# Optimization experiments

Hardware: AMD Instinct MI355X
Metric: run time of the kernel (lower is better)

Reference implementation:

```python
import jax, jax.numpy as jnp
import numpy as np

BZ, T, D, DFF, E, BEAMS = 128, 32, 768, 3072, 8, 2


def setup_inputs() -> dict:
    key = jax.random.key(0)
    ks = jax.random.split(key, 4)
    s = 0.02
    return {
        "x": jax.random.normal(ks[0], (BZ, T, D), jnp.float32),
        "attention_mask": jnp.ones((BZ, T), jnp.float32),
        "Wg": jax.random.normal(ks[1], (D, E), jnp.float32) * s,   # gate Linear(D,E,bias=False)
        "W1": jax.random.normal(ks[2], (E, D, DFF), jnp.float32) * s,
        "b1": jnp.zeros((E, DFF), jnp.float32),
        "W2": jax.random.normal(ks[3], (E, DFF, D), jnp.float32) * s,
        "b2": jnp.zeros((E, D), jnp.float32),
    }


def reference(x, attention_mask, Wg, W1, b1, W2, b2):
    # forward_gate: module builds its own all-ones mask regardless of input mask
    mask = jnp.ones((x.shape[0], x.shape[1]), x.dtype)
    x_avg = (x * mask[..., None]).sum(1) / mask[..., None].sum(1)   # [bz, D]
    prob = jax.nn.softmax(x_avg @ Wg, axis=-1)                       # [bz, E]
    # beam_search (layer_judge='first', pre-route): topk on exp(log(softmax)) == softmax probs
    scores = jnp.exp(jnp.log(prob))
    topv, topi = jax.lax.top_k(scores, BEAMS)                        # [bz, beams]
    beam_scores = topv.reshape(-1)                                   # [bz*beams]
    expert_route = topi.reshape(-1, 1)                                # [bz*beams, 1]
    sel = expert_route[:, -1]
    # replicate x per beam: [bz*beams, T, D]
    x_rep = jnp.broadcast_to(x[:, None], (x.shape[0], BEAMS, x.shape[1], x.shape[2]))
    x_rep = x_rep.reshape(-1, x.shape[1], x.shape[2])
    # per-sample expert FFN dispatch (dense masked loop over the E=8 experts)
    out = jnp.zeros_like(x_rep)
    for e in range(E):
        h = jax.nn.gelu(jnp.einsum('nsd,df->nsf', x_rep, W1[e]) + b1[e], approximate=False)
        ye = jnp.einsum('nsf,fd->nsd', h, W2[e]) + b2[e]
        out = jnp.where((sel == e)[:, None, None], ye, out)
    return (out, beam_scores, expert_route)
```

## Files before the change

### kernel.cpp

```cpp
#include <hip/hip_runtime.h>
#include <cstddef>
#include <cstdint>

#define BZd   128
#define Td    32
#define Dd    768
#define DFFd  3072
#define Ed    8
#define NBEAM 256
#define ROWS_TOT 8192
#define OUT_ELEMS 6291456
#define MAXTILES 72

typedef unsigned short u16;
typedef __attribute__((ext_vector_type(4))) unsigned short ushort4v;
typedef __attribute__((ext_vector_type(8))) short frag_ab;
typedef __attribute__((ext_vector_type(4))) float floatx4;

__device__ __forceinline__ u16 f2bf(float f) {
  unsigned int u = __builtin_bit_cast(unsigned int, f);
  u += 0x7FFFu + ((u >> 16) & 1u);
  return (u16)(u >> 16);
}

__device__ __forceinline__ void async_copy16(u16* lds, const u16* g) {
  __builtin_amdgcn_global_load_lds(
      (const __attribute__((address_space(1))) void*)g,
      (__attribute__((address_space(3))) void*)lds, 16, 0, 0);
}

__device__ __forceinline__ float gelu_fast(float x) {
  float z = 1.5957691216f * (x + 0.044715f * x * x * x);
  return x / (1.0f + __expf(-z));
}

__global__ __launch_bounds__(256) void route_kernel(
    const float* __restrict__ x, const float* __restrict__ Wg,
    float* __restrict__ out, int* __restrict__ sel) {
  int b = blockIdx.x;
  int t = threadIdx.x;
  __shared__ float red[256][8];
  float la[8];
#pragma unroll
  for (int e = 0; e < 8; e++) la[e] = 0.f;
  for (int d = t; d < Dd; d += 256) {
    const float* xp = x + (size_t)b * Td * Dd + d;
    float xa = 0.f;
#pragma unroll
    for (int tt = 0; tt < Td; tt++) xa += xp[(size_t)tt * Dd];
    xa *= (1.0f / 32.0f);
#pragma unroll
    for (int e = 0; e < 8; e++) la[e] += xa * Wg[d * 8 + e];
  }
#pragma unroll
  for (int e = 0; e < 8; e++) red[t][e] = la[e];
  __syncthreads();
  for (int s = 128; s > 0; s >>= 1) {
    if (t < s) {
#pragma unroll
      for (int e = 0; e < 8; e++) red[t][e] += red[t + s][e];
    }
    __syncthreads();
  }
  if (t == 0) {
    float lg[8];
#pragma unroll
    for (int e = 0; e < 8; e++) lg[e] = red[0][e];
    float mx = lg[0];
#pragma unroll
    for (int e = 1; e < 8; e++) mx = fmaxf(mx, lg[e]);
    float p[8];
    float sum = 0.f;
#pragma unroll
    for (int e = 0; e < 8; e++) { p[e] = __expf(lg[e] - mx); sum += p[e]; }
    float inv = 1.0f / sum;
#pragma unroll
    for (int e = 0; e < 8; e++) p[e] *= inv;
    int i0 = 0; float v0 = p[0];
#pragma unroll
    for (int e = 1; e < 8; e++) if (p[e] > v0) { v0 = p[e]; i0 = e; }
    int i1 = -1; float v1 = -1.0f;
#pragma unroll
    for (int e = 0; e < 8; e++) if (e != i0 && p[e] > v1) { v1 = p[e]; i1 = e; }
    float* bs = out + OUT_ELEMS;
    float* er = out + OUT_ELEMS + NBEAM;
    bs[2 * b] = v0; bs[2 * b + 1] = v1;
    er[2 * b] = (float)i0; er[2 * b + 1] = (float)i1;
    sel[2 * b] = i0; sel[2 * b + 1] = i1;
  }
}

__global__ __launch_bounds__(256) void bucket_kernel(
    const int* __restrict__ sel, int* __restrict__ perm, int4* __restrict__ tiles) {
  __shared__ int ssel[NBEAM];
  __shared__ int scnt[8];
  __shared__ int soff[8];
  __shared__ int scur[8];
  __shared__ int sperm[NBEAM];
  int t = threadIdx.x;
  ssel[t] = sel[t];
  __syncthreads();
  if (t == 0) {
    for (int e = 0; e < 8; e++) scnt[e] = 0;
    for (int n = 0; n < NBEAM; n++) scnt[ssel[n]]++;
    int o = 0;
    for (int e = 0; e < 8; e++) { soff[e] = o; scur[e] = o; o += scnt[e]; }
    for (int n = 0; n < NBEAM; n++) { int e = ssel[n]; sperm[scur[e]++] = n; }
    int tt = 0;
    for (int e = 0; e < 8; e++) {
      int nr = scnt[e] * 32;
      int base = soff[e] * 32;
      for (int r0 = 0; r0 < nr; r0 += 128) {
        tiles[tt] = make_int4(e, base + r0, min(128, nr - r0), 0);
        tt++;
      }
    }
    for (; tt < MAXTILES; tt++) tiles[tt] = make_int4(-1, 0, 0, 0);
  }
  __syncthreads();
  perm[t] = sperm[t];
}

__global__ __launch_bounds__(256) void convert_x_kernel(
    const float* __restrict__ x, u16* __restrict__ xbf) {
  size_t i = ((size_t)blockIdx.x * 256 + threadIdx.x) * 4;
  float4 v = *(const float4*)(x + i);
  ushort4v pv = {f2bf(v.x), f2bf(v.y), f2bf(v.z), f2bf(v.w)};
  *(ushort4v*)(xbf + i) = pv;
}

__global__ __launch_bounds__(256) void transpose_bf16_kernel(
    const float* __restrict__ in, u16* __restrict__ out, int row0, int col0,
    int ld_in, size_t estr_in, int ld_out, size_t estr_out) {
  __shared__ u16 tile[64][65];
  int e = blockIdx.z;
  int r0 = blockIdx.x * 64, c0 = blockIdx.y * 64;
  int t = threadIdx.x;
  int rr = t >> 4, cc4 = (t & 15) * 4;
  const float* ip = in + (size_t)e * estr_in + (size_t)(row0 + r0) * ld_in + col0 + c0;
#pragma unroll
  for (int i = 0; i < 4; i++) {
    int r = rr + 16 * i;
    float4 v = *(const float4*)(ip + (size_t)r * ld_in + cc4);
    tile[r][cc4 + 0] = f2bf(v.x);
    tile[r][cc4 + 1] = f2bf(v.y);
    tile[r][cc4 + 2] = f2bf(v.z);
    tile[r][cc4 + 3] = f2bf(v.w);
  }
  __syncthreads();
  int ccw = t >> 4, r4 = (t & 15) * 4;
  u16* op = out + (size_t)e * estr_out + (size_t)c0 * ld_out + r0;
#pragma unroll
  for (int i = 0; i < 4; i++) {
    int cc = ccw + 16 * i;
    ushort4v pv = {tile[r4 + 0][cc], tile[r4 + 1][cc], tile[r4 + 2][cc], tile[r4 + 3][cc]};
    *(ushort4v*)(op + (size_t)cc * ld_out + r4) = pv;
  }
}

__global__ __launch_bounds__(256) void gemm1_kernel(
    const u16* __restrict__ xbf, const u16* __restrict__ w1t,
    const float* __restrict__ b1, const int* __restrict__ perm,
    const int4* __restrict__ tiles, u16* __restrict__ h, int f0, int FC) {
  int4 meta = tiles[blockIdx.y];
  int e = meta.x;
  if (e < 0) return;
  int grow0 = meta.y, nrows = meta.z;
  int bx = blockIdx.x;

  __shared__ __align__(16) u16 As[128 * 64];
  __shared__ __align__(16) u16 Bs[128 * 64];

  int t = threadIdx.x;
  int l = t & 63, w = t >> 6;
  int wm = w & 1, wn = w >> 1;
  int lrow = l & 15, lquad = l >> 4;

  const u16* ag[4]; const u16* bg[4];
  u16* al[4]; u16* bl[4];
#pragma unroll
  for (int j = 0; j < 4; j++) {
    int s = j * 256 + t;
    int m = s >> 3;
    int koff = (((s & 7) ^ ((m >> 1) & 7))) * 8;
    int bidx = (grow0 >> 5) + (m >> 5);
    bidx = bidx < NBEAM ? bidx : NBEAM - 1;
    int batch = perm[bidx] >> 1;
    ag[j] = xbf + ((size_t)batch * Td + (m & 31)) * Dd + koff;
    bg[j] = w1t + ((size_t)e * FC + bx * 128 + m) * Dd + koff;
    al[j] = As + j * 2048 + w * 512;
    bl[j] = Bs + j * 2048 + w * 512;
  }

  int aoff[2][4], boff[2][4];
#pragma unroll
  for (int hh = 0; hh < 2; hh++)
#pragma unroll
    for (int i = 0; i < 4; i++) {
      int ra = wm * 64 + i * 16 + lrow;
      aoff[hh][i] = ra * 64 + (((lquad + hh * 4) ^ ((ra >> 1) & 7)) * 8);
      int rb = wn * 64 + i * 16 + lrow;
      boff[hh][i] = rb * 64 + (((lquad + hh * 4) ^ ((rb >> 1) & 7)) * 8);
    }

  floatx4 acc[4][4];
#pragma unroll
  for (int mi = 0; mi < 4; mi++)
#pragma unroll
    for (int ni = 0; ni < 4; ni++) acc[mi][ni] = (floatx4){0.f, 0.f, 0.f, 0.f};

  for (int kt = 0; kt < Dd; kt += 64) {
#pragma unroll
    for (int j = 0; j < 4; j++) {
      async_copy16(al[j], ag[j]);
      async_copy16(bl[j], bg[j]);
      ag[j] += 64; bg[j] += 64;
    }
    __syncthreads();
#pragma unroll
    for (int hh = 0; hh < 2; hh++) {
      frag_ab af[4], bf[4];
#pragma unroll
      for (int mi = 0; mi < 4; mi++) af[mi] = *(const frag_ab*)(As + aoff[hh][mi]);
#pragma unroll
      for (int ni = 0; ni < 4; ni++) bf[ni] = *(const frag_ab*)(Bs + boff[hh][ni]);
#pragma unroll
      for (int mi = 0; mi < 4; mi++)
#pragma unroll
        for (int ni = 0; ni < 4; ni++)
          acc[mi][ni] = __builtin_amdgcn_mfma_f32_16x16x32_bf16(af[mi], bf[ni], acc[mi][ni], 0, 0, 0);
    }
    __syncthreads();
  }

  int f_base = bx * 128;
#pragma unroll
  for (int mi = 0; mi < 4; mi++) {
    int row0 = wm * 64 + mi * 16 + lquad * 4;
#pragma unroll
    for (int ni = 0; ni < 4; ni++) {
      int col = wn * 64 + ni * 16 + lrow;
      float bias = b1[(size_t)e * DFFd + f0 + f_base + col];
#pragma unroll
      for (int r = 0; r < 4; r++) {
        int row = row0 + r;
        if (row < nrows) {
          float vv = acc[mi][ni][r] + bias;
          h[(size_t)(grow0 + row) * FC + f_base + col] = f2bf(gelu_fast(vv));
        }
      }
    }
  }
}

__global__ __launch_bounds__(256) void gemm2_kernel(
    const u16* __restrict__ h, const u16* __restrict__ w2t,
    const float* __restrict__ b2, const int* __restrict__ perm,
    const int4* __restrict__ tiles, float* __restrict__ out,
    int FC, int first) {
  int4 meta = tiles[blockIdx.y];
  int e = meta.x;
  if (e < 0) return;
  int grow0 = meta.y, nrows = meta.z;
  int bx = blockIdx.x;

  __shared__ __align__(16) u16 As[128 * 64];
  __shared__ __align__(16) u16 Bs[128 * 64];
  __shared__ int sbeam[4];

  int t = threadIdx.x;
  if (t < 4) {
    int idx = (grow0 >> 5) + t;
    sbeam[t] = perm[idx < NBEAM ? idx : NBEAM - 1];
  }
  int l = t & 63, w = t >> 6;
  int wm = w & 1, wn = w >> 1;
  int lrow = l & 15, lquad = l >> 4;

  const u16* ag[4]; const u16* bg[4];
  u16* al[4]; u16* bl[4];
#pragma unroll
  for (int j = 0; j < 4; j++) {
    int s = j * 256 + t;
    int m = s >> 3;
    int koff = (((s & 7) ^ ((m >> 1) & 7))) * 8;
    int arow = grow0 + m;
    arow = arow < ROWS_TOT ? arow : ROWS_TOT - 1;
    ag[j] = h + (size_t)arow * FC + koff;
    bg[j] = w2t + ((size_t)e * Dd + bx * 128 + m) * FC + koff;
    al[j] = As + j * 2048 + w * 512;
    bl[j] = Bs + j * 2048 + w * 512;
  }

  int aoff[2][4], boff[2][4];
#pragma unroll
  for (int hh = 0; hh < 2; hh++)
#pragma unroll
    for (int i = 0; i < 4; i++) {
      int ra = wm * 64 + i * 16 + lrow;
      aoff[hh][i] = ra * 64 + (((lquad + hh * 4) ^ ((ra >> 1) & 7)) * 8);
      int rb = wn * 64 + i * 16 + lrow;
      boff[hh][i] = rb * 64 + (((lquad + hh * 4) ^ ((rb >> 1) & 7)) * 8);
    }

  floatx4 acc[4][4];
#pragma unroll
  for (int mi = 0; mi < 4; mi++)
#pragma unroll
    for (int ni = 0; ni < 4; ni++) acc[mi][ni] = (floatx4){0.f, 0.f, 0.f, 0.f};

  for (int kt = 0; kt < FC; kt += 64) {
#pragma unroll
    for (int j = 0; j < 4; j++) {
      async_copy16(al[j], ag[j]);
      async_copy16(bl[j], bg[j]);
      ag[j] += 64; bg[j] += 64;
    }
    __syncthreads();
#pragma unroll
    for (int hh = 0; hh < 2; hh++) {
      frag_ab af[4], bf[4];
#pragma unroll
      for (int mi = 0; mi < 4; mi++) af[mi] = *(const frag_ab*)(As + aoff[hh][mi]);
#pragma unroll
      for (int ni = 0; ni < 4; ni++) bf[ni] = *(const frag_ab*)(Bs + boff[hh][ni]);
#pragma unroll
      for (int mi = 0; mi < 4; mi++)
#pragma unroll
        for (int ni = 0; ni < 4; ni++)
          acc[mi][ni] = __builtin_amdgcn_mfma_f32_16x16x32_bf16(af[mi], bf[ni], acc[mi][ni], 0, 0, 0);
    }
    __syncthreads();
  }

#pragma unroll
  for (int mi = 0; mi < 4; mi++) {
    int row0 = wm * 64 + mi * 16 + lquad * 4;
#pragma unroll
    for (int ni = 0; ni < 4; ni++) {
      int col = wn * 64 + ni * 16 + lrow;
      int dg = bx * 128 + col;
      float bias = b2[(size_t)e * Dd + dg];
#pragma unroll
      for (int r = 0; r < 4; r++) {
        int row = row0 + r;
        if (row < nrows) {
          int beam = sbeam[row >> 5];
          size_t o = ((size_t)beam * Td + (row & 31)) * Dd + dg;
          if (first) out[o] = acc[mi][ni][r] + bias;
          else out[o] += acc[mi][ni][r];
        }
      }
    }
  }
}

extern "C" void kernel_launch(void* const* d_in, const int* in_sizes, int n_in,
                              void* d_out, int out_size, void* d_ws, size_t ws_size,
                              hipStream_t stream) {
  const float* x  = (const float*)d_in[0];
  const float* Wg = (const float*)d_in[2];
  const float* W1 = (const float*)d_in[3];
  const float* b1 = (const float*)d_in[4];
  const float* W2 = (const float*)d_in[5];
  const float* b2 = (const float*)d_in[6];
  float* out = (float*)d_out;

  char* ws = (char*)d_ws;
  int*  sel   = (int*)ws;
  int*  perm  = sel + NBEAM;
  int4* tiles = (int4*)(ws + 4096);

  const size_t xbf_off = 65536;
  const size_t xbf_bytes = (size_t)BZd * Td * Dd * 2;
  int FC = 384;
  if      (xbf_off + xbf_bytes + (size_t)40960 * 3072 <= ws_size) FC = 3072;
  else if (xbf_off + xbf_bytes + (size_t)40960 * 1536 <= ws_size) FC = 1536;
  else if (xbf_off + xbf_bytes + (size_t)40960 * 768  <= ws_size) FC = 768;
  int NC = DFFd / FC;

  u16* xbf = (u16*)(ws + xbf_off);
  u16* w1t = (u16*)(ws + xbf_off + xbf_bytes);
  u16* w2t = w1t + (size_t)Ed * FC * Dd;
  u16* h   = w2t + (size_t)Ed * Dd * FC;

  route_kernel<<<BZd, 256, 0, stream>>>(x, Wg, out, sel);
  bucket_kernel<<<1, 256, 0, stream>>>(sel, perm, tiles);
  convert_x_kernel<<<(BZd * Td * Dd) / 1024, 256, 0, stream>>>(x, xbf);

  for (int c = 0; c < NC; c++) {
    transpose_bf16_kernel<<<dim3(Dd / 64, FC / 64, Ed), 256, 0, stream>>>(
        W1, w1t, 0, c * FC, DFFd, (size_t)Dd * DFFd, Dd, (size_t)FC * Dd);
    transpose_bf16_kernel<<<dim3(FC / 64, Dd / 64, Ed), 256, 0, stream>>>(
        W2, w2t, c * FC, 0, Dd, (size_t)DFFd * Dd, FC, (size_t)Dd * FC);
    gemm1_kernel<<<dim3(FC / 128, MAXTILES), 256, 0, stream>>>(
        xbf, w1t, b1, perm, tiles, h, c * FC, FC);
    gemm2_kernel<<<dim3(Dd / 128, MAXTILES), 256, 0, stream>>>(
        h, w2t, b2, perm, tiles, out, FC, c == 0 ? 1 : 0);
  }
}
```

Before: 396.2 us.

## Double-buffer LDS tiles in expert GEMMs and vectorize epilogue stores

Both expert GEMM kernels now use two LDS buffers. The next K-tile is issued with global_load_lds while the current one feeds the MFMAs, with a manual vmcnt wait plus barrier in place of two __syncthreads per iteration. MFMA operands are swapped so each lane holds four consecutive output columns, which lets the bias add, GELU and stores run as vector float4/ushort4 accesses instead of scalar ones. s_setprio is raised around the MFMA block. LDS use doubles to 64KB per block, which may reduce occupancy.

```diff
diff --git a/kernel.cpp b/kernel.cpp
--- a/kernel.cpp
+++ b/kernel.cpp
@@ -32,6 +32,18 @@
 __device__ __forceinline__ float gelu_fast(float x) {
   float z = 1.5957691216f * (x + 0.044715f * x * x * x);
   return x / (1.0f + __expf(-z));
+}
+
+__device__ __forceinline__ void stage8(u16* const (&al)[4], u16* const (&bl)[4],
+                                       const u16* (&ag)[4], const u16* (&bg)[4],
+                                       int off) {
+#pragma unroll
+  for (int j = 0; j < 4; j++) {
+    async_copy16(al[j] + off, ag[j]);
+    async_copy16(bl[j] + off, bg[j]);
+    ag[j] += 64;
+    bg[j] += 64;
+  }
 }
 
 __global__ __launch_bounds__(256) void route_kernel(
@@ -168,8 +180,8 @@
   int grow0 = meta.y, nrows = meta.z;
   int bx = blockIdx.x;
 
-  __shared__ __align__(16) u16 As[128 * 64];
-  __shared__ __align__(16) u16 Bs[128 * 64];
+  __shared__ __align__(16) u16 As[2 * 128 * 64];
+  __shared__ __align__(16) u16 Bs[2 * 128 * 64];
 
   int t = threadIdx.x;
   int l = t & 63, w = t >> 6;
@@ -209,45 +221,52 @@
 #pragma unroll
     for (int ni = 0; ni < 4; ni++) acc[mi][ni] = (floatx4){0.f, 0.f, 0.f, 0.f};
 
-  for (int kt = 0; kt < Dd; kt += 64) {
-#pragma unroll
-    for (int j = 0; j < 4; j++) {
-      async_copy16(al[j], ag[j]);
-      async_copy16(bl[j], bg[j]);
-      ag[j] += 64; bg[j] += 64;
-    }
-    __syncthreads();
+  const int nk = Dd / 64;
+  stage8(al, bl, ag, bg, 0);
+
+  for (int kt = 0; kt < nk; kt++) {
+    const int cur = kt & 1;
+    if (kt + 1 < nk) {
+      stage8(al, bl, ag, bg, (cur ^ 1) * 8192);
+      asm volatile("s_waitcnt vmcnt(8)\n\ts_barrier" ::: "memory");
+    } else {
+      asm volatile("s_waitcnt vmcnt(0)\n\ts_barrier" ::: "memory");
+    }
+    const u16* Ab = As + cur * 8192;
+    const u16* Bb = Bs + cur * 8192;
 #pragma unroll
     for (int hh = 0; hh < 2; hh++) {
-      frag_ab af[4], bf[4];
-#pragma unroll
-      for (int mi = 0; mi < 4; mi++) af[mi] = *(const frag_ab*)(As + aoff[hh][mi]);
-#pragma unroll
-      for (int ni = 0; ni < 4; ni++) bf[ni] = *(const frag_ab*)(Bs + boff[hh][ni]);
+      frag_ab af[4], bfr[4];
+#pragma unroll
+      for (int mi = 0; mi < 4; mi++) af[mi] = *(const frag_ab*)(Ab + aoff[hh][mi]);
+#pragma unroll
+      for (int ni = 0; ni < 4; ni++) bfr[ni] = *(const frag_ab*)(Bb + boff[hh][ni]);
+      __builtin_amdgcn_s_setprio(1);
 #pragma unroll
       for (int mi = 0; mi < 4; mi++)
 #pragma unroll
         for (int ni = 0; ni < 4; ni++)
-          acc[mi][ni] = __builtin_amdgcn_mfma_f32_16x16x32_bf16(af[mi], bf[ni], acc[mi][ni], 0, 0, 0);
-    }
-    __syncthreads();
+          acc[mi][ni] = __builtin_amdgcn_mfma_f32_16x16x32_bf16(bfr[ni], af[mi], acc[mi][ni], 0, 0, 0);
+      __builtin_amdgcn_s_setprio(0);
+    }
+    asm volatile("s_barrier" ::: "memory");
   }
 
   int f_base = bx * 128;
 #pragma unroll
   for (int mi = 0; mi < 4; mi++) {
-    int row0 = wm * 64 + mi * 16 + lquad * 4;
-#pragma unroll
-    for (int ni = 0; ni < 4; ni++) {
-      int col = wn * 64 + ni * 16 + lrow;
-      float bias = b1[(size_t)e * DFFd + f0 + f_base + col];
-#pragma unroll
-      for (int r = 0; r < 4; r++) {
-        int row = row0 + r;
-        if (row < nrows) {
-          float vv = acc[mi][ni][r] + bias;
-          h[(size_t)(grow0 + row) * FC + f_base + col] = f2bf(gelu_fast(vv));
-        }
+    int row = wm * 64 + mi * 16 + lrow;
+    if (row < nrows) {
+      u16* hp = h + (size_t)(grow0 + row) * FC + f_base + wn * 64 + lquad * 4;
+      const float* bp = b1 + (size_t)e * DFFd + f0 + f_base + wn * 64 + lquad * 4;
+#pragma unroll
+      for (int ni = 0; ni < 4; ni++) {
+        float4 bias = *(const float4*)(bp + ni * 16);
+        ushort4v pv = {f2bf(gelu_fast(acc[mi][ni][0] + bias.x)),
+                       f2bf(gelu_fast(acc[mi][ni][1] + bias.y)),
+                       f2bf(gelu_fast(acc[mi][ni][2] + bias.z)),
+                       f2bf(gelu_fast(acc[mi][ni][3] + bias.w))};
+        *(ushort4v*)(hp + ni * 16) = pv;
       }
     }
   }
@@ -264,8 +283,8 @@
   int grow0 = meta.y, nrows = meta.z;
   int bx = blockIdx.x;
 
-  __shared__ __align__(16) u16 As[128 * 64];
-  __shared__ __align__(16) u16 Bs[128 * 64];
+  __shared__ __align__(16) u16 As[2 * 128 * 64];
+  __shared__ __align__(16) u16 Bs[2 * 128 * 64];
   __shared__ int sbeam[4];
 
   int t = threadIdx.x;
@@ -273,6 +292,8 @@
     int idx = (grow0 >> 5) + t;
     sbeam[t] = perm[idx < NBEAM ? idx : NBEAM - 1];
   }
+  __syncthreads();
+
   int l = t & 63, w = t >> 6;
   int wm = w & 1, wn = w >> 1;
   int lrow = l & 15, lquad = l >> 4;
@@ -309,46 +330,57 @@
 #pragma unroll
     for (int ni = 0; ni < 4; ni++) acc[mi][ni] = (floatx4){0.f, 0.f, 0.f, 0.f};
 
-  for (int kt = 0; kt < FC; kt += 64) {
-#pragma unroll
-    for (int j = 0; j < 4; j++) {
-      async_copy16(al[j], ag[j]);
-      async_copy16(bl[j], bg[j]);
-      ag[j] += 64; bg[j] += 64;
-    }
-    __syncthreads();
+  const int nk = FC / 64;
+  stage8(al, bl, ag, bg, 0);
+
+#pragma unroll 2
+  for (int kt = 0; kt < nk; kt++) {
+    const int cur = kt & 1;
+    if (kt + 1 < nk) {
+      stage8(al, bl, ag, bg, (cur ^ 1) * 8192);
+      asm volatile("s_waitcnt vmcnt(8)\n\ts_barrier" ::: "memory");
+    } else {
+      asm volatile("s_waitcnt vmcnt(0)\n\ts_barrier" ::: "memory");
+    }
+    const u16* Ab = As + cur * 8192;
+    const u16* Bb = Bs + cur * 8192;
 #pragma unroll
     for (int hh = 0; hh < 2; hh++) {
-      frag_ab af[4], bf[4];
-#pragma unroll
-      for (int mi = 0; mi < 4; mi++) af[mi] = *(const frag_ab*)(As + aoff[hh][mi]);
-#pragma unroll
-      for (int ni = 0; ni < 4; ni++) bf[ni] = *(const frag_ab*)(Bs + boff[hh][ni]);
+      frag_ab af[4], bfr[4];
+#pragma unroll
+      for (int mi = 0; mi < 4; mi++) af[mi] = *(const frag_ab*)(Ab + aoff[hh][mi]);
+#pragma unroll
+      for (int ni = 0; ni < 4; ni++) bfr[ni] = *(const frag_ab*)(Bb + boff[hh][ni]);
+      __builtin_amdgcn_s_setprio(1);
 #pragma unroll
       for (int mi = 0; mi < 4; mi++)
 #pragma unroll
         for (int ni = 0; ni < 4; ni++)
-          acc[mi][ni] = __builtin_amdgcn_mfma_f32_16x16x32_bf16(af[mi], bf[ni], acc[mi][ni], 0, 0, 0);
-    }
-    __syncthreads();
+          acc[mi][ni] = __builtin_amdgcn_mfma_f32_16x16x32_bf16(bfr[ni], af[mi], acc[mi][ni], 0, 0, 0);
+      __builtin_amdgcn_s_setprio(0);
+    }
+    asm volatile("s_barrier" ::: "memory");
   }
 
 #pragma unroll
   for (int mi = 0; mi < 4; mi++) {
-    int row0 = wm * 64 + mi * 16 + lquad * 4;
-#pragma unroll
-    for (int ni = 0; ni < 4; ni++) {
-      int col = wn * 64 + ni * 16 + lrow;
-      int dg = bx * 128 + col;
-      float bias = b2[(size_t)e * Dd + dg];
-#pragma unroll
-      for (int r = 0; r < 4; r++) {
-        int row = row0 + r;
-        if (row < nrows) {
-          int beam = sbeam[row >> 5];
-          size_t o = ((size_t)beam * Td + (row & 31)) * Dd + dg;
-          if (first) out[o] = acc[mi][ni][r] + bias;
-          else out[o] += acc[mi][ni][r];
+    int row = wm * 64 + mi * 16 + lrow;
+    if (row < nrows) {
+      int beam = sbeam[row >> 5];
+      float* op = out + ((size_t)beam * Td + (row & 31)) * Dd + bx * 128 + wn * 64 + lquad * 4;
+      const float* bp = b2 + (size_t)e * Dd + bx * 128 + wn * 64 + lquad * 4;
+#pragma unroll
+      for (int ni = 0; ni < 4; ni++) {
+        if (first) {
+          float4 bias = *(const float4*)(bp + ni * 16);
+          float4 v = {acc[mi][ni][0] + bias.x, acc[mi][ni][1] + bias.y,
+                      acc[mi][ni][2] + bias.z, acc[mi][ni][3] + bias.w};
+          *(float4*)(op + ni * 16) = v;
+        } else {
+          float4 o = *(float4*)(op + ni * 16);
+          o.x += acc[mi][ni][0]; o.y += acc[mi][ni][1];
+          o.z += acc[mi][ni][2]; o.w += acc[mi][ni][3];
+          *(float4*)(op + ni * 16) = o;
         }
       }
     }
```

Measured after the change: 379.5 us. -4.2%, faster.
